# Kernel tuning notes

Measured on AMD Instinct MI355X. Metric: run time of the kernel, lower is better.

Reference implementation:

```python
import jax, jax.numpy as jnp
import numpy as np

KERNEL_SIZE = 16
STRIDE = 8
NEG = -1.0e9


def setup_inputs() -> dict:
    key = jax.random.key(0)
    k1, k2, k3, k4, k5 = jax.random.split(key, 5)
    B, C, L = 8, 512, 4096
    x = jax.random.normal(k1, (B, C, L), dtype=jnp.float32)
    mask = jax.random.randint(k2, (B, L), 0, 2).astype(bool)
    W = jax.random.normal(k3, (C, C), dtype=jnp.float32) * 0.02
    b = jax.random.normal(k4, (C,), dtype=jnp.float32) * 0.02
    v = jax.random.normal(k5, (C,), dtype=jnp.float32) * 0.02
    return {"x": x, "mask": mask, "W": W, "b": b, "v": v}


def reference(x, mask, W, b, v):
    # x: [B, C, L], mask: [B, L] (True = masked out)
    B, C, L = x.shape
    win, step = KERNEL_SIZE, STRIDE
    L_pool = 1 + (L - win) // step
    # per-token projection (identical across windows since proj is per-token)
    h = jnp.tanh(jnp.einsum('bcl,dc->bld', x, W) + b)      # [B, L, C]
    s = jnp.einsum('bld,d->bl', h, v)                       # [B, L]
    idx = jnp.arange(L_pool)[:, None] * step + jnp.arange(win)[None, :]
    sw = s[:, idx]
    mw = mask[:, idx]
    sw = jnp.where(mw, NEG, sw)
    w = jax.nn.softmax(sw, axis=-1)
    w = jnp.where(mw, 0.0, w)
    norm = jnp.clip(jnp.sum(w, axis=-1, keepdims=True), 1e-6, None)
    w = w / norm
    xw = x[:, :, idx]
    return jnp.einsum('bcpw,bpw->bcp', xw, w)               # [B, C, L_pool]
```

## Files before the change

kernel.cpp:

```cpp
#include <hip/hip_runtime.h>
#include <hip/hip_bf16.h>
#include <cmath>

#define Bsz 8
#define Csz 512
#define Lsz 4096
#define LPOOL 511
#define NEGV -1000000000.0f

typedef __attribute__((ext_vector_type(8))) short short8;
typedef __attribute__((ext_vector_type(4))) float float4v;

__device__ __forceinline__ float bf2f(short u) {
  unsigned int x = ((unsigned int)(unsigned short)u) << 16;
  return __builtin_bit_cast(float, x);
}

__global__ __launch_bounds__(256) void prep(const unsigned char* __restrict__ mb,
    int* __restrict__ flag, const float* __restrict__ W,
    __hip_bfloat16* __restrict__ Wts) {
  const int bid = blockIdx.x, tid = threadIdx.x;
  if (bid == 0) {
    __shared__ int sf;
    if (tid == 0) sf = 0;
    __syncthreads();
    int f = 0;
    for (int i = tid; i < 4096; i += 256)
      if ((i & 3) && mb[i]) f = 1;
    if (f) atomicOr(&sf, 1);
    __syncthreads();
    if (tid == 0) *flag = sf;
  } else {
    int tg = (bid - 1) * 256 + tid;
    int d = tg >> 6, cg = tg & 63;
    float4 w0 = *(const float4*)(W + (size_t)d * 512 + cg * 8);
    float4 w1 = *(const float4*)(W + (size_t)d * 512 + cg * 8 + 4);
    __hip_bfloat16 hb[8];
    hb[0] = __float2bfloat16(w0.x); hb[1] = __float2bfloat16(w0.y);
    hb[2] = __float2bfloat16(w0.z); hb[3] = __float2bfloat16(w0.w);
    hb[4] = __float2bfloat16(w1.x); hb[5] = __float2bfloat16(w1.y);
    hb[6] = __float2bfloat16(w1.z); hb[7] = __float2bfloat16(w1.w);
    int nt = d >> 7, row = d & 127, ks = cg >> 2, seg = cg & 3;
    *(short8*)(Wts + (((size_t)nt * 16 + ks) * 512 + seg * 128 + row) * 8) = *(short8*)hb;
  }
}

__global__ __launch_bounds__(256, 2) void gemm_fused(
    const float* __restrict__ x, const __hip_bfloat16* __restrict__ Wts,
    const float* __restrict__ bias, const float* __restrict__ v,
    float* __restrict__ s) {
  __shared__ short8 aU[4096];
  __shared__ float sX[32][65];
  __shared__ float s_acc[64];
  const int tid = threadIdx.x;
  const int lane = tid & 63, wave = tid >> 6;
  const int lr = lane & 15, quad = lane >> 4;
  const int bid = blockIdx.x;
  const int b = bid >> 6, l0 = (bid & 63) * 64;

  if (tid < 64) s_acc[tid] = 0.f;

  float bl[8], vl[8];
  #pragma unroll
  for (int nf = 0; nf < 8; ++nf) {
    int n = wave * 128 + nf * 16 + lr;
    bl[nf] = bias[n]; vl[nf] = v[n];
  }

  float4v acc[4][8];
  #pragma unroll
  for (int i = 0; i < 4; ++i)
    #pragma unroll
    for (int j = 0; j < 8; ++j) acc[i][j] = (float4v)0.f;

  const float* xb = x + ((size_t)b * Csz) * Lsz + l0;
  const int cl = tid >> 4;
  const int l4 = (tid & 15) * 4;
  const int cg = tid >> 6;
  const int ll = tid & 63;
  for (int cc = 0; cc < 16; ++cc) {
    #pragma unroll
    for (int it = 0; it < 2; ++it) {
      int c = it * 16 + cl;
      *(float4*)(&sX[c][l4]) = *(const float4*)(xb + (size_t)(cc * 32 + c) * Lsz + l4);
    }
    __syncthreads();
    __hip_bfloat16 hb[8];
    #pragma unroll
    for (int j = 0; j < 8; ++j)
      hb[j] = __float2bfloat16(sX[cg * 8 + j][ll]);
    aU[cc * 256 + cg * 64 + ll] = *(short8*)hb;
    __syncthreads();
  }

  const short8* bBase = (const short8*)Wts + (size_t)wave * 8192 + quad * 128 + lr;
  for (int ks = 0; ks < 16; ++ks) {
    short8 af[4];
    #pragma unroll
    for (int mf = 0; mf < 4; ++mf)
      af[mf] = aU[ks * 256 + quad * 64 + mf * 16 + lr];
    short8 bfr[8];
    #pragma unroll
    for (int nf = 0; nf < 8; ++nf)
      bfr[nf] = bBase[(size_t)ks * 512 + nf * 16];
    #pragma unroll
    for (int mf = 0; mf < 4; ++mf)
      #pragma unroll
      for (int nf = 0; nf < 8; ++nf)
        acc[mf][nf] = __builtin_amdgcn_mfma_f32_16x16x32_bf16(af[mf], bfr[nf], acc[mf][nf], 0, 0, 0);
  }

  __syncthreads();
  #pragma unroll
  for (int mf = 0; mf < 4; ++mf) {
    #pragma unroll
    for (int reg = 0; reg < 4; ++reg) {
      float p = 0.f;
      #pragma unroll
      for (int nf = 0; nf < 8; ++nf)
        p += tanhf(acc[mf][nf][reg] + bl[nf]) * vl[nf];
      p += __shfl_xor(p, 1, 16);
      p += __shfl_xor(p, 2, 16);
      p += __shfl_xor(p, 4, 16);
      p += __shfl_xor(p, 8, 16);
      if (lr == 0)
        atomicAdd(&s_acc[mf * 16 + quad * 4 + reg], p);
    }
  }
  __syncthreads();
  if (tid < 64) s[(size_t)bid * 64 + tid] = s_acc[tid];
}

__global__ __launch_bounds__(256) void pool2(const float* __restrict__ x,
    const float* __restrict__ s, const void* __restrict__ mask,
    const int* __restrict__ flag, float* __restrict__ out) {
  __shared__ float wl[8][17];
  const int t = threadIdx.x;
  const int p0 = blockIdx.x * 8, b = blockIdx.y;
  if (t < 8 && p0 + t < LPOOL) {
    const int p = p0 + t;
    const bool u8 = (*flag != 0);
    const unsigned char* m8 = (const unsigned char*)mask;
    const int* m32 = (const int*)mask;
    const int base = b * Lsz + p * 8;
    float sv[16]; int mv[16];
    float mx = -3.4e38f;
    #pragma unroll
    for (int w = 0; w < 16; ++w) {
      int mk = u8 ? (int)m8[base + w] : m32[base + w];
      float val = mk ? NEGV : s[base + w];
      sv[w] = val; mv[w] = mk;
      mx = fmaxf(mx, val);
    }
    float sum = 0.f;
    #pragma unroll
    for (int w = 0; w < 16; ++w) { sv[w] = expf(sv[w] - mx); sum += sv[w]; }
    float inv = 1.0f / sum;
    float norm = 0.f;
    #pragma unroll
    for (int w = 0; w < 16; ++w) { sv[w] = mv[w] ? 0.f : sv[w] * inv; norm += sv[w]; }
    norm = fmaxf(norm, 1e-6f);
    float rn = 1.0f / norm;
    #pragma unroll
    for (int w = 0; w < 16; ++w) wl[t][w] = sv[w] * rn;
  }
  __syncthreads();
  const int ci = t >> 3, pi = t & 7;
  const int p = p0 + pi;
  if (p >= LPOOL) return;
  float wr[16];
  #pragma unroll
  for (int w = 0; w < 16; ++w) wr[w] = wl[pi][w];
  #pragma unroll 4
  for (int it = 0; it < 16; ++it) {
    int c = it * 32 + ci;
    const float* xp = x + ((size_t)b * Csz + c) * Lsz + 8 * p;
    float acc = 0.f;
    #pragma unroll
    for (int q = 0; q < 4; ++q) {
      float4 xv = *(const float4*)(xp + q * 4);
      acc += xv.x * wr[q * 4] + xv.y * wr[q * 4 + 1] +
             xv.z * wr[q * 4 + 2] + xv.w * wr[q * 4 + 3];
    }
    out[((size_t)b * Csz + c) * LPOOL + p] = acc;
  }
}

__global__ void detect_mask(const unsigned char* __restrict__ mb, int* __restrict__ flag) {
  __shared__ int sf;
  int t = threadIdx.x;
  if (t == 0) sf = 0;
  __syncthreads();
  int f = 0;
  for (int i = t; i < 4096; i += 256)
    if ((i & 3) && mb[i]) f = 1;
  if (f) atomicOr(&sf, 1);
  __syncthreads();
  if (t == 0) *flag = sf;
}

__global__ __launch_bounds__(256) void gemm_s_f32(const float* __restrict__ x,
    const float* __restrict__ W, const float* __restrict__ bias,
    const float* __restrict__ v, float* __restrict__ s_out) {
  __shared__ float sA[32][64];
  __shared__ float sB[32][68];
  __shared__ float s_acc[64];
  const int tid = threadIdx.x;
  const int b = blockIdx.y;
  const int l0 = blockIdx.x * 64;
  if (tid < 64) s_acc[tid] = 0.0f;
  const int tx = tid & 15;
  const int ty = tid >> 4;
  const float* xb = x + ((size_t)b * Csz) * Lsz + l0;
  for (int d0 = 0; d0 < Csz; d0 += 64) {
    float acc[4][4] = {{0.f}};
    for (int c0 = 0; c0 < Csz; c0 += 32) {
      __syncthreads();
      #pragma unroll
      for (int it = 0; it < 8; ++it) {
        int idx = tid + it * 256;
        int kc = idx >> 6, ml = idx & 63;
        sA[kc][ml] = xb[(size_t)(c0 + kc) * Lsz + ml];
      }
      #pragma unroll
      for (int it = 0; it < 8; ++it) {
        int idx = tid + it * 256;
        int kc = idx & 31, dj = idx >> 5;
        sB[kc][dj] = W[(size_t)(d0 + dj) * Csz + c0 + kc];
      }
      __syncthreads();
      #pragma unroll
      for (int kc = 0; kc < 32; ++kc) {
        float4 a  = *(const float4*)(&sA[kc][tx << 2]);
        float4 w4 = *(const float4*)(&sB[kc][ty << 2]);
        acc[0][0] += a.x * w4.x; acc[0][1] += a.x * w4.y; acc[0][2] += a.x * w4.z; acc[0][3] += a.x * w4.w;
        acc[1][0] += a.y * w4.x; acc[1][1] += a.y * w4.y; acc[1][2] += a.y * w4.z; acc[1][3] += a.y * w4.w;
        acc[2][0] += a.z * w4.x; acc[2][1] += a.z * w4.y; acc[2][2] += a.z * w4.z; acc[2][3] += a.z * w4.w;
        acc[3][0] += a.w * w4.x; acc[3][1] += a.w * w4.y; acc[3][2] += a.w * w4.z; acc[3][3] += a.w * w4.w;
      }
    }
    float part[4] = {0.f, 0.f, 0.f, 0.f};
    #pragma unroll
    for (int j = 0; j < 4; ++j) {
      int d = d0 + (ty << 2) + j;
      float bj = bias[d], vj = v[d];
      #pragma unroll
      for (int i = 0; i < 4; ++i)
        part[i] += tanhf(acc[i][j] + bj) * vj;
    }
    #pragma unroll
    for (int i = 0; i < 4; ++i)
      atomicAdd(&s_acc[(tx << 2) + i], part[i]);
  }
  __syncthreads();
  if (tid < 64) s_out[(size_t)b * Lsz + l0 + tid] = s_acc[tid];
}

__global__ void win_weights(const float* __restrict__ s, const void* __restrict__ mask,
                            const int* __restrict__ flag, float* __restrict__ wgt) {
  int t = blockIdx.x * blockDim.x + threadIdx.x;
  if (t >= Bsz * LPOOL) return;
  int b = t / LPOOL, p = t - b * LPOOL;
  const bool u8 = (*flag != 0);
  const unsigned char* m8 = (const unsigned char*)mask;
  const int* m32 = (const int*)mask;
  float sv[16]; int mv[16];
  float mx = -3.4e38f;
  int base = b * Lsz + p * 8;
  #pragma unroll
  for (int w = 0; w < 16; ++w) {
    int mk = u8 ? (int)m8[base + w] : m32[base + w];
    float val = mk ? NEGV : s[base + w];
    sv[w] = val; mv[w] = mk;
    mx = fmaxf(mx, val);
  }
  float sum = 0.f;
  #pragma unroll
  for (int w = 0; w < 16; ++w) { sv[w] = expf(sv[w] - mx); sum += sv[w]; }
  float inv = 1.0f / sum;
  float norm = 0.f;
  #pragma unroll
  for (int w = 0; w < 16; ++w) { sv[w] = mv[w] ? 0.f : sv[w] * inv; norm += sv[w]; }
  norm = fmaxf(norm, 1e-6f);
  float rn = 1.0f / norm;
  #pragma unroll
  for (int w = 0; w < 16; ++w) wgt[t * 16 + w] = sv[w] * rn;
}

__global__ __launch_bounds__(256) void pool_out(const float* __restrict__ x,
    const float* __restrict__ wgt, float* __restrict__ out) {
  __shared__ float xrow[Lsz];
  int bc = blockIdx.x;
  int c = bc & (Csz - 1);
  int b = bc >> 9;
  const float* xr = x + ((size_t)b * Csz + c) * Lsz;
  int tid = threadIdx.x;
  #pragma unroll
  for (int it = 0; it < 4; ++it) {
    int idx = (tid + it * 256) << 2;
    *(float4*)(&xrow[idx]) = *(const float4*)(&xr[idx]);
  }
  __syncthreads();
  const float* wb = wgt + (size_t)b * LPOOL * 16;
  float* ob = out + ((size_t)b * Csz + c) * LPOOL;
  for (int p = tid; p < LPOOL; p += 256) {
    const float4* wp = (const float4*)(wb + p * 16);
    const float4* xp = (const float4*)(&xrow[p * 8]);
    float acc = 0.f;
    #pragma unroll
    for (int q = 0; q < 4; ++q) {
      float4 wv = wp[q], xv = xp[q];
      acc += xv.x * wv.x + xv.y * wv.y + xv.z * wv.z + xv.w * wv.w;
    }
    ob[p] = acc;
  }
}

extern "C" void kernel_launch(void* const* d_in, const int* in_sizes, int n_in,
                              void* d_out, int out_size, void* d_ws, size_t ws_size,
                              hipStream_t stream) {
  const float* x    = (const float*)d_in[0];
  const void*  mask = d_in[1];
  const float* W    = (const float*)d_in[2];
  const float* bias = (const float*)d_in[3];
  const float* v    = (const float*)d_in[4];
  float* out = (float*)d_out;

  char* wsb = (char*)d_ws;
  int*   flag = (int*)wsb;
  float* s    = (float*)(wsb + 512);
  float* wgt  = (float*)(wsb + 131584);
  __hip_bfloat16* Wts = (__hip_bfloat16*)(wsb + 524288);
  const size_t NEED = 524288 + 524288;

  if (ws_size >= NEED) {
    prep<<<129, 256, 0, stream>>>((const unsigned char*)mask, flag, W, Wts);
    gemm_fused<<<512, 256, 0, stream>>>(x, Wts, bias, v, s);
    pool2<<<dim3(64, Bsz), 256, 0, stream>>>(x, s, mask, flag, out);
  } else {
    detect_mask<<<1, 256, 0, stream>>>((const unsigned char*)mask, flag);
    gemm_s_f32<<<dim3(Lsz / 64, Bsz), 256, 0, stream>>>(x, W, bias, v, s);
    win_weights<<<(Bsz * LPOOL + 255) / 256, 256, 0, stream>>>(s, mask, flag, wgt);
    pool_out<<<Bsz * Csz, 256, 0, stream>>>(x, wgt, out);
  }
}
```

Baseline: 161.6 us.

## Shrink GEMM tile, double-buffer x staging, and use fast tanh

The fused projection GEMM drops from 64 to 32 tokens per block and doubles the grid to 1024 blocks. It replaces the upfront staging of all 512 channels into LDS with a two-buffer pipeline that prefetches the next 32-channel slab from global memory while MFMAs run on the current one. Launch bounds now ask for 4 blocks per CU, and tanhf is swapped for an exp-based approximation. The goal is higher occupancy and overlap of x loads with compute, at the cost of more per-slab syncs, twice as many W fragment reads across blocks, and slightly different tanh numerics.

```diff
diff --git a/kernel.cpp b/kernel.cpp
--- a/kernel.cpp
+++ b/kernel.cpp
@@ -14,6 +14,11 @@
 __device__ __forceinline__ float bf2f(short u) {
   unsigned int x = ((unsigned int)(unsigned short)u) << 16;
   return __builtin_bit_cast(float, x);
+}
+
+__device__ __forceinline__ float tanh_fast(float x) {
+  float e = __expf(2.0f * x);
+  return 1.0f - 2.0f / (e + 1.0f);
 }
 
 __global__ __launch_bounds__(256) void prep(const unsigned char* __restrict__ mb,
@@ -45,20 +50,20 @@
   }
 }
 
-__global__ __launch_bounds__(256, 2) void gemm_fused(
+__global__ __launch_bounds__(256, 4) void gemm_fused(
     const float* __restrict__ x, const __hip_bfloat16* __restrict__ Wts,
     const float* __restrict__ bias, const float* __restrict__ v,
     float* __restrict__ s) {
-  __shared__ short8 aU[4096];
-  __shared__ float sX[32][65];
-  __shared__ float s_acc[64];
+  __shared__ short8 aU[2][128];
+  __shared__ float sX[32][33];
+  __shared__ float s_acc[32];
   const int tid = threadIdx.x;
   const int lane = tid & 63, wave = tid >> 6;
   const int lr = lane & 15, quad = lane >> 4;
   const int bid = blockIdx.x;
-  const int b = bid >> 6, l0 = (bid & 63) * 64;
-
-  if (tid < 64) s_acc[tid] = 0.f;
+  const int b = bid >> 7, l0 = (bid & 127) * 32;
+
+  if (tid < 32) s_acc[tid] = 0.f;
 
   float bl[8], vl[8];
   #pragma unroll
@@ -67,58 +72,71 @@
     bl[nf] = bias[n]; vl[nf] = v[n];
   }
 
-  float4v acc[4][8];
-  #pragma unroll
-  for (int i = 0; i < 4; ++i)
+  float4v acc[2][8];
+  #pragma unroll
+  for (int i = 0; i < 2; ++i)
     #pragma unroll
     for (int j = 0; j < 8; ++j) acc[i][j] = (float4v)0.f;
 
-  const float* xb = x + ((size_t)b * Csz) * Lsz + l0;
-  const int cl = tid >> 4;
-  const int l4 = (tid & 15) * 4;
-  const int cg = tid >> 6;
-  const int ll = tid & 63;
-  for (int cc = 0; cc < 16; ++cc) {
-    #pragma unroll
-    for (int it = 0; it < 2; ++it) {
-      int c = it * 16 + cl;
-      *(float4*)(&sX[c][l4]) = *(const float4*)(xb + (size_t)(cc * 32 + c) * Lsz + l4);
-    }
+  const int xc = tid >> 3, xl = (tid & 7) * 4;
+  const float* xb = x + ((size_t)b * Csz + xc) * Lsz + l0 + xl;
+  const int pcg = tid >> 5, pll = tid & 31;
+  const short8* bBase = (const short8*)Wts + (size_t)wave * 8192 + quad * 128 + lr;
+
+  float4 cur = *(const float4*)(xb);
+  sX[xc][xl] = cur.x; sX[xc][xl + 1] = cur.y;
+  sX[xc][xl + 2] = cur.z; sX[xc][xl + 3] = cur.w;
+  __syncthreads();
+  if (tid < 128) {
+    __hip_bfloat16 hb[8];
+    #pragma unroll
+    for (int j = 0; j < 8; ++j)
+      hb[j] = __float2bfloat16(sX[pcg * 8 + j][pll]);
+    aU[0][pcg * 32 + pll] = *(short8*)hb;
+  }
+  float4 nxt = *(const float4*)(xb + (size_t)32 * Lsz);
+
+  int buf = 0;
+  for (int ks = 0; ks < 16; ++ks) {
     __syncthreads();
-    __hip_bfloat16 hb[8];
-    #pragma unroll
-    for (int j = 0; j < 8; ++j)
-      hb[j] = __float2bfloat16(sX[cg * 8 + j][ll]);
-    aU[cc * 256 + cg * 64 + ll] = *(short8*)hb;
-    __syncthreads();
-  }
-
-  const short8* bBase = (const short8*)Wts + (size_t)wave * 8192 + quad * 128 + lr;
-  for (int ks = 0; ks < 16; ++ks) {
-    short8 af[4];
-    #pragma unroll
-    for (int mf = 0; mf < 4; ++mf)
-      af[mf] = aU[ks * 256 + quad * 64 + mf * 16 + lr];
+    if (ks < 15) {
+      sX[xc][xl] = nxt.x; sX[xc][xl + 1] = nxt.y;
+      sX[xc][xl + 2] = nxt.z; sX[xc][xl + 3] = nxt.w;
+      if (ks < 14)
+        nxt = *(const float4*)(xb + (size_t)(ks + 2) * 32 * Lsz);
+    }
     short8 bfr[8];
     #pragma unroll
     for (int nf = 0; nf < 8; ++nf)
       bfr[nf] = bBase[(size_t)ks * 512 + nf * 16];
-    #pragma unroll
-    for (int mf = 0; mf < 4; ++mf)
+    short8 af[2];
+    #pragma unroll
+    for (int mf = 0; mf < 2; ++mf)
+      af[mf] = aU[buf][quad * 32 + mf * 16 + lr];
+    #pragma unroll
+    for (int mf = 0; mf < 2; ++mf)
       #pragma unroll
       for (int nf = 0; nf < 8; ++nf)
         acc[mf][nf] = __builtin_amdgcn_mfma_f32_16x16x32_bf16(af[mf], bfr[nf], acc[mf][nf], 0, 0, 0);
-  }
-
-  __syncthreads();
-  #pragma unroll
-  for (int mf = 0; mf < 4; ++mf) {
+    __syncthreads();
+    if (ks < 15 && tid < 128) {
+      __hip_bfloat16 hb[8];
+      #pragma unroll
+      for (int j = 0; j < 8; ++j)
+        hb[j] = __float2bfloat16(sX[pcg * 8 + j][pll]);
+      aU[buf ^ 1][pcg * 32 + pll] = *(short8*)hb;
+    }
+    buf ^= 1;
+  }
+
+  #pragma unroll
+  for (int mf = 0; mf < 2; ++mf) {
     #pragma unroll
     for (int reg = 0; reg < 4; ++reg) {
       float p = 0.f;
       #pragma unroll
       for (int nf = 0; nf < 8; ++nf)
-        p += tanhf(acc[mf][nf][reg] + bl[nf]) * vl[nf];
+        p += tanh_fast(acc[mf][nf][reg] + bl[nf]) * vl[nf];
       p += __shfl_xor(p, 1, 16);
       p += __shfl_xor(p, 2, 16);
       p += __shfl_xor(p, 4, 16);
@@ -128,7 +146,7 @@
     }
   }
   __syncthreads();
-  if (tid < 64) s[(size_t)bid * 64 + tid] = s_acc[tid];
+  if (tid < 32) s[(size_t)bid * 32 + tid] = s_acc[tid];
 }
 
 __global__ __launch_bounds__(256) void pool2(const float* __restrict__ x,
@@ -335,7 +353,7 @@
 
   if (ws_size >= NEED) {
     prep<<<129, 256, 0, stream>>>((const unsigned char*)mask, flag, W, Wts);
-    gemm_fused<<<512, 256, 0, stream>>>(x, Wts, bias, v, s);
+    gemm_fused<<<1024, 256, 0, stream>>>(x, Wts, bias, v, s);
     pool2<<<dim3(64, Bsz), 256, 0, stream>>>(x, s, mask, flag, out);
   } else {
     detect_mask<<<1, 256, 0, stream>>>((const unsigned char*)mask, flag);
```

Measured after the change: 171.3 us. +6.0%, slower.
